# Performance work log

Hardware: AMD Instinct MI355X
Metric: run time of the kernel (lower is better)

The kernel has to match this reference:

```python
import jax, jax.numpy as jnp
import numpy as np

D_MODEL = 1024
NUM_HEADS = 16
HEAD_DIM = D_MODEL // NUM_HEADS          # 64
ROT_W = HEAD_DIM // 2                    # partial_factor=(0.0, 0.5) -> rotary on first half
MAX_LEN = 2048
BASE = 10000.0


def _rope_tables(max_len):
    # theta over even dims of ROT_W, each repeated twice (interleaved pairs): [t0,t0,t1,t1,...]
    theta = 1.0 / (BASE ** (np.arange(0, ROT_W, 2, dtype=np.float32) / ROT_W))  # [ROT_W/2]
    m = np.arange(max_len, dtype=np.float32)[:, None] * theta[None, :]          # [max_len, ROT_W/2]
    m = np.repeat(m, 2, axis=-1)                                                # [max_len, ROT_W]
    return jnp.asarray(np.cos(m)), jnp.asarray(np.sin(m))


def _rotate(x):
    # interleaved pairs (x0, x1) -> (-x1, x0)
    xr = x.reshape(x.shape[:-1] + (-1, 2))
    rot = jnp.stack([-xr[..., 1], xr[..., 0]], axis=-1)
    return rot.reshape(x.shape)


def setup_inputs() -> dict:
    key = jax.random.key(0)
    k1, k2, k3, k4 = jax.random.split(key, 4)
    B, L, H, E = 2, 2048, NUM_HEADS, HEAD_DIM
    return {
        "queries": jax.random.normal(k1, (B, L, H, E), jnp.float32),
        "keys": jax.random.normal(k2, (B, L, H, E), jnp.float32),
        "values": jax.random.normal(k3, (B, L, H, E), jnp.float32),
        "bias_weight": jax.random.normal(k4, (2, H), jnp.float32) * 0.02,  # BinaryAttentionBias embedding
        "n_vars": 32,
        "n_tokens": 64,
    }


def reference(queries, keys, values, bias_weight, n_vars, n_tokens):
    B, L, H, E = queries.shape
    q = queries.transpose(0, 2, 1, 3)  # [B,H,L,E]
    k = keys.transpose(0, 2, 1, 3)     # [B,H,L,E]

    # --- partial rotary projection (shared for q and k), seq_id = arange(L) ---
    cos, sin = _rope_tables(MAX_LEN)
    seq = jnp.arange(n_vars * n_tokens)
    c = cos[seq][None, None]  # [1,1,L,ROT_W]
    s = sin[seq][None, None]

    def rope(x):
        xr = x[..., :ROT_W]
        return jnp.concatenate([c * xr + s * _rotate(xr), x[..., ROT_W:]], axis=-1)

    q = rope(q)
    k = rope(k)

    scale = 1.0 / np.sqrt(E).astype(np.float32)

    # --- binary attention bias: per-head scalar by variable-id equality ---
    var_id = jnp.repeat(jnp.arange(n_vars), n_tokens)          # [L]
    same_var = var_id[:, None] == var_id[None, :]              # [L,L]
    bias = jnp.where(same_var[None, :, :],
                     bias_weight[1][:, None, None],
                     bias_weight[0][:, None, None])            # [H,L,L]

    # --- TimerMultivariateMask: causal in time, full across variables ---
    time_id = seq % n_tokens
    causal_bad = time_id[None, :] > time_id[:, None]           # key time > query time
    attn_mask = jnp.where(causal_bad[None], -jnp.inf, bias)    # [H,L,L]

    scores = jnp.einsum('bhle,bhse->bhls', q, k)               # [B,H,L,L]
    A = jax.nn.softmax(scale * scores + attn_mask[None], axis=-1)
    V = jnp.einsum('bhls,bshd->blhd', A, values)               # [B,L,H,E]
    return V
```

## Files before the change

kernel.cpp:

```cpp
#include <hip/hip_runtime.h>

typedef unsigned short u16;
typedef unsigned int u32;

typedef __attribute__((ext_vector_type(8))) __bf16 bf16x8;
typedef __attribute__((ext_vector_type(4))) float floatx4;

#define B_ 2
#define L_ 2048
#define H_ 16
#define E_ 64
#define QK_ELEMS (B_ * H_ * L_ * E_)
#define WS_OFF 128

static __device__ __forceinline__ float bf2f(u16 v) {
  u32 u = ((u32)v) << 16;
  return __builtin_bit_cast(float, u);
}
static __device__ __forceinline__ u16 f2bf(float x) {
  u32 u = __builtin_bit_cast(u32, x);
  u32 r = (u + 0x7FFFu + ((u >> 16) & 1u)) >> 16;
  return (u16)r;
}

static __device__ __forceinline__ float exp2_fast(float x) {
  float r;
  asm("v_exp_f32 %0, %1" : "=v"(r) : "v"(x));
  return r;
}

static __device__ __forceinline__ void sincos_fast(float a, float* s, float* c) {
  const float INV2PI = 0.15915494309189535f;
  float r = a * INV2PI;
  r = r - floorf(r);
  float ss, cc;
  asm("v_sin_f32 %0, %1" : "=v"(ss) : "v"(r));
  asm("v_cos_f32 %0, %1" : "=v"(cc) : "v"(r));
  *s = ss;
  *c = cc;
}

static __device__ __forceinline__ bool detect_f32_wave(const void* q) {
  u32 w = ((const u32*)q)[threadIdx.x & 63];
  int big = ((((w >> 7) & 0xFF) > 180) | (((w >> 23) & 0xFF) > 180));
  return __ballot(big) != 0ULL;
}

__global__ void detect_dtype(const u16* __restrict__ q, int* __restrict__ flag) {
  int lane = threadIdx.x;
  int big = 0;
#pragma unroll
  for (int i = 0; i < 16; ++i) {
    u16 v = q[lane * 16 + i];
    int e = (v >> 7) & 0xFF;
    big |= (e > 180);
  }
  unsigned long long b = __ballot(big);
  if (lane == 0) *flag = (b != 0ULL) ? 1 : 0;
}

static __device__ __forceinline__ bf16x8 ld8(const void* base, size_t off, bool f32) {
  if (f32) {
    const float* p = (const float*)base + off;
    float4 a = *(const float4*)p;
    float4 bb = *(const float4*)(p + 4);
    uint4 o;
    o.x = (u32)f2bf(a.x) | ((u32)f2bf(a.y) << 16);
    o.y = (u32)f2bf(a.z) | ((u32)f2bf(a.w) << 16);
    o.z = (u32)f2bf(bb.x) | ((u32)f2bf(bb.y) << 16);
    o.w = (u32)f2bf(bb.z) | ((u32)f2bf(bb.w) << 16);
    return __builtin_bit_cast(bf16x8, o);
  }
  return *(const bf16x8*)((const u16*)base + off);
}

static __device__ __forceinline__ bf16x8 rope_frag(bf16x8 x, float pos, int quad) {
  uint4 u = __builtin_bit_cast(uint4, x);
  float v0 = bf2f((u16)u.x), v1 = bf2f((u16)(u.x >> 16));
  float v2 = bf2f((u16)u.y), v3 = bf2f((u16)(u.y >> 16));
  float v4 = bf2f((u16)u.z), v5 = bf2f((u16)(u.z >> 16));
  float v6 = bf2f((u16)u.w), v7 = bf2f((u16)(u.w >> 16));
  const float LB = 0.83048202372184058696f;
  float jb = (float)(quad * 4);
  float a0 = pos * exp2_fast(-jb * LB);
  float a1 = pos * exp2_fast(-(jb + 1.f) * LB);
  float a2 = pos * exp2_fast(-(jb + 2.f) * LB);
  float a3 = pos * exp2_fast(-(jb + 3.f) * LB);
  float s0, c0, s1, c1, s2, c2, s3, c3;
  sincos_fast(a0, &s0, &c0);
  sincos_fast(a1, &s1, &c1);
  sincos_fast(a2, &s2, &c2);
  sincos_fast(a3, &s3, &c3);
  uint4 o;
  o.x = (u32)f2bf(c0 * v0 - s0 * v1) | ((u32)f2bf(c0 * v1 + s0 * v0) << 16);
  o.y = (u32)f2bf(c1 * v2 - s1 * v3) | ((u32)f2bf(c1 * v3 + s1 * v2) << 16);
  o.z = (u32)f2bf(c2 * v4 - s2 * v5) | ((u32)f2bf(c2 * v5 + s2 * v4) << 16);
  o.w = (u32)f2bf(c3 * v6 - s3 * v7) | ((u32)f2bf(c3 * v7 + s3 * v6) << 16);
  return __builtin_bit_cast(bf16x8, o);
}

__global__ __launch_bounds__(256) void prep_kv(
    const void* __restrict__ Q, const void* __restrict__ K, const void* __restrict__ V,
    u16* __restrict__ Kr, u16* __restrict__ VT) {
  __shared__ u16 tile[64][65];
  const int t = threadIdx.x;
  const bool f32 = detect_f32_wave(Q);

  if (blockIdx.x < (B_ * L_)) {
    const int bl = blockIdx.x;
    const int b = bl >> 11, l = bl & (L_ - 1);
    const int h = t >> 4, d = (t & 15) << 2;
    size_t in_off = (((size_t)(b * L_ + l) * H_ + h) * E_) + d;
    size_t out_off = (((size_t)(b * H_ + h) * L_ + l) * E_) + d;
    float k0, k1, k2, k3;
    if (f32) {
      float4 kv = *(const float4*)((const float*)K + in_off);
      k0 = kv.x; k1 = kv.y; k2 = kv.z; k3 = kv.w;
    } else {
      uint2 kv = *(const uint2*)((const u16*)K + in_off);
      k0 = bf2f((u16)kv.x); k1 = bf2f((u16)(kv.x >> 16));
      k2 = bf2f((u16)kv.y); k3 = bf2f((u16)(kv.y >> 16));
    }
    if (d < 32) {
      int j0 = d >> 1;
      const float LB = 0.83048202372184058696f;
      float a0 = (float)l * exp2_fast(-(float)j0 * LB);
      float a1 = (float)l * exp2_fast(-(float)(j0 + 1) * LB);
      float s0, c0, s1, c1;
      sincos_fast(a0, &s0, &c0);
      sincos_fast(a1, &s1, &c1);
      float r;
      r = c0 * k0 - s0 * k1; k1 = c0 * k1 + s0 * k0; k0 = r;
      r = c1 * k2 - s1 * k3; k3 = c1 * k3 + s1 * k2; k2 = r;
    }
    uint2 ko;
    ko.x = (u32)f2bf(k0) | ((u32)f2bf(k1) << 16);
    ko.y = (u32)f2bf(k2) | ((u32)f2bf(k3) << 16);
    *(uint2*)(Kr + out_off) = ko;
  } else {
    const int blk = blockIdx.x - (B_ * L_);
    const int bh = blk & 31, lt = blk >> 5;
    const int b = bh >> 4, h = bh & 15;
    const int l0 = lt << 6;
#pragma unroll
    for (int it = 0; it < 2; ++it) {
      int ll = (t >> 3) + (it << 5);
      int dc = (t & 7) << 3;
      size_t off = (((size_t)(b * L_ + l0 + ll) * H_ + h) * E_) + dc;
      bf16x8 x8 = ld8(V, off, f32);
      uint4 x = __builtin_bit_cast(uint4, x8);
      tile[ll][dc + 0] = (u16)x.x; tile[ll][dc + 1] = (u16)(x.x >> 16);
      tile[ll][dc + 2] = (u16)x.y; tile[ll][dc + 3] = (u16)(x.y >> 16);
      tile[ll][dc + 4] = (u16)x.z; tile[ll][dc + 5] = (u16)(x.z >> 16);
      tile[ll][dc + 6] = (u16)x.w; tile[ll][dc + 7] = (u16)(x.w >> 16);
    }
    __syncthreads();
    int e = t >> 2, lg = (t & 3) << 4;
    u32 pk[8];
#pragma unroll
    for (int i = 0; i < 8; ++i)
      pk[i] = (u32)tile[lg + 2 * i][e] | ((u32)tile[lg + 2 * i + 1][e] << 16);
    u16* dst = VT + (((size_t)bh * E_ + e) * L_) + l0 + lg;
    uint4 o0; o0.x = pk[0]; o0.y = pk[1]; o0.z = pk[2]; o0.w = pk[3];
    uint4 o1; o1.x = pk[4]; o1.y = pk[5]; o1.z = pk[6]; o1.w = pk[7];
    *(uint4*)dst = o0;
    *(uint4*)(dst + 8) = o1;
  }
}

#if __has_builtin(__builtin_amdgcn_global_load_lds)
#define HAS_GLL 1
static __device__ __forceinline__ void gll16(const void* g, void* l) {
  __builtin_amdgcn_global_load_lds(
      (const __attribute__((address_space(1))) u32*)g,
      (__attribute__((address_space(3))) u32*)l, 16, 0, 0);
}
#else
#define HAS_GLL 0
#endif

__global__ __launch_bounds__(256, 2) void flash_staged(
    const void* __restrict__ Q, const u16* __restrict__ Kr,
    const u16* __restrict__ VT, const void* __restrict__ bw,
    void* __restrict__ out) {
  __shared__ u16 kbuf[2][64][64];
  __shared__ u16 vbuf[2][64][64];
  __shared__ u16 plds[4][2][32 * 36];

  const int tid = threadIdx.x;
  const int wid = tid >> 6, lane = tid & 63;
  const int quad = lane >> 4, l16 = lane & 15;
  const int bh = blockIdx.x & 31;
  const int gb = blockIdx.x >> 5;
  const int var_l = (gb << 1) + (wid >> 1);
  const int s0 = (wid & 1) << 4;
  const int base = var_l << 6;
  const int b = bh >> 4, h = bh & 15;

  const bool f32 = detect_f32_wave(Q);
  const u16* Kb = Kr + ((size_t)bh << 17);
  const u16* Vb = VT + ((size_t)bh << 17);

  const float LOG2E = 1.4426950408889634f;
  const float bw_diff = f32 ? ((const float*)bw)[h] : bf2f(((const u16*)bw)[h]);
  const float bw_same = f32 ? ((const float*)bw)[H_ + h] : bf2f(((const u16*)bw)[H_ + h]);
  const float C1 = 0.125f * LOG2E;
  const float c2d = bw_diff * LOG2E;
  const float c2s = bw_same * LOG2E;
  const float NEGINF = -__builtin_inff();

  bf16x8 qf[2][2];
#pragma unroll
  for (int rh = 0; rh < 2; ++rh) {
    const int r = base + s0 + (rh << 5) + l16;
    size_t ro = (((size_t)(b * L_ + r) * H_ + h) * E_);
    qf[rh][0] = rope_frag(ld8(Q, ro + quad * 8, f32), (float)r, quad);
    qf[rh][1] = ld8(Q, ro + 32 + quad * 8, f32);
  }

  const floatx4 zero4 = {0.f, 0.f, 0.f, 0.f};
  bf16x8 ones;
  { uint4 t4; t4.x = t4.y = t4.z = t4.w = 0x3F803F80u; ones = __builtin_bit_cast(bf16x8, t4); }

  floatx4 oacc[2][4], lacc[2];
#pragma unroll
  for (int rh = 0; rh < 2; ++rh) {
    lacc[rh] = zero4;
#pragma unroll
    for (int c4 = 0; c4 < 4; ++c4) oacc[rh][c4] = zero4;
  }

  const int srow = lane >> 3;
  const int sc16 = (lane & 7) ^ srow;
#if !HAS_GLL
  uint4 sk[2], sv[2];
#endif
  auto stage_issue = [&](int bufn, int v) {
    const int k0 = v << 6;
#pragma unroll
    for (int rr = 0; rr < 2; ++rr) {
      const int chunk = (wid << 1) + rr;
      const int row = (chunk << 3) + srow;
      const u16* gk = Kb + (size_t)(k0 + row) * 64 + sc16 * 8;
      const u16* gv = Vb + (size_t)row * L_ + (size_t)k0 + sc16 * 8;
#if HAS_GLL
      gll16(gk, (char*)&kbuf[bufn][0][0] + chunk * 1024);
      gll16(gv, (char*)&vbuf[bufn][0][0] + chunk * 1024);
#else
      sk[rr] = *(const uint4*)gk;
      sv[rr] = *(const uint4*)gv;
#endif
    }
  };
  auto stage_commit = [&](int bufn) {
#if !HAS_GLL
#pragma unroll
    for (int rr = 0; rr < 2; ++rr) {
      const int chunk = (wid << 1) + rr;
      *(uint4*)((u16*)&kbuf[bufn][0][0] + chunk * 512 + lane * 8) = sk[rr];
      *(uint4*)((u16*)&vbuf[bufn][0][0] + chunk * 512 + lane * 8) = sv[rr];
    }
#else
    (void)bufn;
#endif
  };

  stage_issue(0, 0);
  stage_commit(0);
  __asm__ volatile("s_waitcnt vmcnt(0)" ::: "memory");
  __syncthreads();

  int pp = 0;
  const int sw = l16 & 7;

  for (int v = 0; v < 32; ++v) {
    const int buf = v & 1;
    const bool more = (v < 31);
    if (more) stage_issue(buf ^ 1, v + 1);
    const float c2 = (v == var_l) ? c2s : c2d;

    bf16x8 kf[2][2];
#pragma unroll
    for (int ch = 0; ch < 2; ++ch) {
      const int row = ch * 16 + l16;
#pragma unroll
      for (int hf = 0; hf < 2; ++hf)
        kf[ch][hf] = *(const bf16x8*)&kbuf[buf][row][(((hf << 2) + quad) ^ sw) << 3];
    }
    floatx4 cc[2][2];
#pragma unroll
    for (int rh = 0; rh < 2; ++rh)
#pragma unroll
      for (int ch = 0; ch < 2; ++ch) {
        floatx4 acc = __builtin_amdgcn_mfma_f32_16x16x32_bf16(qf[rh][0], kf[ch][0], zero4, 0, 0, 0);
        cc[rh][ch] = __builtin_amdgcn_mfma_f32_16x16x32_bf16(qf[rh][1], kf[ch][1], acc, 0, 0, 0);
      }
    u16* const pw = &plds[wid][pp][0];
#pragma unroll
    for (int rh = 0; rh < 2; ++rh)
#pragma unroll
      for (int ch = 0; ch < 2; ++ch)
#pragma unroll
        for (int reg = 0; reg < 4; ++reg) {
          float s = fmaf(cc[rh][ch][reg], C1, c2);
          if (rh == 0 && (ch * 16 + l16 > s0 + quad * 4 + reg)) s = NEGINF;
          pw[(rh * 16 + quad * 4 + reg) * 36 + ch * 16 + l16] = f2bf(exp2_fast(s));
        }
    __asm__ volatile("s_waitcnt lgkmcnt(0)" ::: "memory");
    bf16x8 pa[2];
#pragma unroll
    for (int rh = 0; rh < 2; ++rh) {
      const u16* pr = pw + (rh * 16 + l16) * 36 + quad * 8;
      uint2 lo = *(const uint2*)pr;
      uint2 hi = *(const uint2*)(pr + 4);
      uint4 cmb; cmb.x = lo.x; cmb.y = lo.y; cmb.z = hi.x; cmb.w = hi.y;
      pa[rh] = __builtin_bit_cast(bf16x8, cmb);
    }
#pragma unroll
    for (int rh = 0; rh < 2; ++rh)
      lacc[rh] = __builtin_amdgcn_mfma_f32_16x16x32_bf16(pa[rh], ones, lacc[rh], 0, 0, 0);
#pragma unroll
    for (int c4 = 0; c4 < 4; ++c4) {
      bf16x8 vf = *(const bf16x8*)&vbuf[buf][c4 * 16 + l16][(quad ^ sw) << 3];
#pragma unroll
      for (int rh = 0; rh < 2; ++rh)
        oacc[rh][c4] = __builtin_amdgcn_mfma_f32_16x16x32_bf16(pa[rh], vf, oacc[rh][c4], 0, 0, 0);
    }
    pp ^= 1;

    bf16x8 kg[2][2];
#pragma unroll
    for (int ch = 0; ch < 2; ++ch) {
      const int row = 32 + ch * 16 + l16;
#pragma unroll
      for (int hf = 0; hf < 2; ++hf)
        kg[ch][hf] = *(const bf16x8*)&kbuf[buf][row][(((hf << 2) + quad) ^ sw) << 3];
    }
    floatx4 dd[2];
#pragma unroll
    for (int ch = 0; ch < 2; ++ch) {
      floatx4 acc = __builtin_amdgcn_mfma_f32_16x16x32_bf16(qf[1][0], kg[ch][0], zero4, 0, 0, 0);
      dd[ch] = __builtin_amdgcn_mfma_f32_16x16x32_bf16(qf[1][1], kg[ch][1], acc, 0, 0, 0);
    }
    u16* const pw2 = &plds[wid][pp][0];
#pragma unroll
    for (int ch = 0; ch < 2; ++ch)
#pragma unroll
      for (int reg = 0; reg < 4; ++reg) {
        float s = fmaf(dd[ch][reg], C1, c2);
        if (ch * 16 + l16 > s0 + quad * 4 + reg) s = NEGINF;
        pw2[(16 + quad * 4 + reg) * 36 + ch * 16 + l16] = f2bf(exp2_fast(s));
      }
    __asm__ volatile("s_waitcnt lgkmcnt(0)" ::: "memory");
    bf16x8 pb;
    {
      const u16* pr = pw2 + (16 + l16) * 36 + quad * 8;
      uint2 lo = *(const uint2*)pr;
      uint2 hi = *(const uint2*)(pr + 4);
      uint4 cmb; cmb.x = lo.x; cmb.y = lo.y; cmb.z = hi.x; cmb.w = hi.y;
      pb = __builtin_bit_cast(bf16x8, cmb);
    }
    lacc[1] = __builtin_amdgcn_mfma_f32_16x16x32_bf16(pb, ones, lacc[1], 0, 0, 0);
#pragma unroll
    for (int c4 = 0; c4 < 4; ++c4) {
      bf16x8 vf = *(const bf16x8*)&vbuf[buf][c4 * 16 + l16][(((4 + quad) ^ sw)) << 3];
      oacc[1][c4] = __builtin_amdgcn_mfma_f32_16x16x32_bf16(pb, vf, oacc[1][c4], 0, 0, 0);
    }
    pp ^= 1;

    if (more) {
      stage_commit(buf ^ 1);
      __asm__ volatile("s_waitcnt vmcnt(0)" ::: "memory");
      __syncthreads();
    }
  }

  float rinv[2][4];
#pragma unroll
  for (int rh = 0; rh < 2; ++rh)
#pragma unroll
    for (int reg = 0; reg < 4; ++reg) {
      float lv = lacc[rh][reg];
      rinv[rh][reg] = (lv > 1e-30f) ? 1.0f / lv : 0.0f;
    }

#pragma unroll
  for (int rh = 0; rh < 2; ++rh)
#pragma unroll
    for (int c4 = 0; c4 < 4; ++c4)
#pragma unroll
      for (int reg = 0; reg < 4; ++reg) {
        const int row = base + s0 + (rh << 5) + quad * 4 + reg;
        const int col = c4 * 16 + l16;
        float val = oacc[rh][c4][reg] * rinv[rh][reg];
        size_t oo = (((size_t)(b * L_ + row)) * H_ + h) * E_ + col;
        if (f32) ((float*)out)[oo] = val;
        else ((u16*)out)[oo] = f2bf(val);
      }
}

__global__ __launch_bounds__(256) void flash_fused(
    const void* __restrict__ Q, const void* __restrict__ K,
    const void* __restrict__ V, const void* __restrict__ bw,
    const int* __restrict__ flag, void* __restrict__ out) {
  __shared__ u16 plds[4][2][32 * 36];
  __shared__ u16 vlds[4][64][40];
  const bool f32 = flag ? (*flag != 0) : true;
  const int tid = threadIdx.x;
  const int wid = tid >> 6, lane = tid & 63;
  const int quad = lane >> 4, l16 = lane & 15;
  const int bh = blockIdx.x & 31;
  const int g = blockIdx.x >> 5;
  const int rowblk = (g << 2) + wid;
  const int row0 = rowblk << 5;
  const int b = bh >> 4, h = bh & 15;
  const int t0 = row0 & 63;
  const int var_l = row0 >> 6;
  const int ktiles = (t0 >> 5) + 1;

  const float bw_diff = f32 ? ((const float*)bw)[h] : bf2f(((const u16*)bw)[h]);
  const float bw_same = f32 ? ((const float*)bw)[H_ + h] : bf2f(((const u16*)bw)[H_ + h]);

  const floatx4 zero4 = {0.f, 0.f, 0.f, 0.f};
  bf16x8 ones;
  { uint4 t4; t4.x = t4.y = t4.z = t4.w = 0x3F803F80u; ones = __builtin_bit_cast(bf16x8, t4); }

  bf16x8 qf[2][2];
#pragma unroll
  for (int rh = 0; rh < 2; ++rh) {
    const int r = row0 + rh * 16 + l16;
    size_t ro = (((size_t)(b * L_ + r) * H_ + h) * E_);
#pragma unroll
    for (int hf = 0; hf < 2; ++hf)
      qf[rh][hf] = ld8(Q, ro + hf * 32 + quad * 8, f32);
    qf[rh][0] = rope_frag(qf[rh][0], (float)r, quad);
  }

  floatx4 oacc[2][4], lacc[2];
#pragma unroll
  for (int rh = 0; rh < 2; ++rh) {
    lacc[rh] = zero4;
#pragma unroll
    for (int c4 = 0; c4 < 4; ++c4) oacc[rh][c4] = zero4;
  }

  u16* const pbase = &plds[wid][0][0];
  u16* const vb = &vlds[wid][0][0];
  int pp = 0;

  for (int v = 0; v < 32; ++v) {
    const float bias = (v == var_l) ? bw_same : bw_diff;
    for (int kt = 0; kt < ktiles; ++kt) {
      const int k0 = (v << 6) + (kt << 5);

      bf16x8 kf[2][2];
#pragma unroll
      for (int ch = 0; ch < 2; ++ch) {
        const int r = k0 + ch * 16 + l16;
        size_t ro = (((size_t)(b * L_ + r) * H_ + h) * E_);
#pragma unroll
        for (int hf = 0; hf < 2; ++hf)
          kf[ch][hf] = ld8(K, ro + hf * 32 + quad * 8, f32);
        kf[ch][0] = rope_frag(kf[ch][0], (float)r, quad);
      }

      floatx4 cc[2][2];
#pragma unroll
      for (int rh = 0; rh < 2; ++rh)
#pragma unroll
        for (int ch = 0; ch < 2; ++ch) {
          floatx4 acc = __builtin_amdgcn_mfma_f32_16x16x32_bf16(qf[rh][0], kf[ch][0], zero4, 0, 0, 0);
          cc[rh][ch] = __builtin_amdgcn_mfma_f32_16x16x32_bf16(qf[rh][1], kf[ch][1], acc, 0, 0, 0);
        }

      u16* const pw = pbase + pp * (32 * 36);
      const int ts_b = (kt << 5) + l16;
#pragma unroll
      for (int rh = 0; rh < 2; ++rh)
#pragma unroll
        for (int ch = 0; ch < 2; ++ch) {
          const int ts = ts_b + ch * 16;
#pragma unroll
          for (int reg = 0; reg < 4; ++reg) {
            const int tl = t0 + rh * 16 + quad * 4 + reg;
            float s = cc[rh][ch][reg] * 0.125f + bias;
            float p = (ts > tl) ? 0.0f : __expf(s);
            pw[(rh * 16 + quad * 4 + reg) * 36 + ch * 16 + l16] = f2bf(p);
          }
        }

#pragma unroll
      for (int it = 0; it < 4; ++it) {
        const int s = (lane >> 3) + it * 8;
        const int dc = (lane & 7) << 3;
        size_t vo = (((size_t)(b * L_ + k0 + s) * H_ + h) * E_) + dc;
        bf16x8 x8 = ld8(V, vo, f32);
        uint4 x = __builtin_bit_cast(uint4, x8);
        vb[(dc + 0) * 40 + s] = (u16)x.x; vb[(dc + 1) * 40 + s] = (u16)(x.x >> 16);
        vb[(dc + 2) * 40 + s] = (u16)x.y; vb[(dc + 3) * 40 + s] = (u16)(x.y >> 16);
        vb[(dc + 4) * 40 + s] = (u16)x.z; vb[(dc + 5) * 40 + s] = (u16)(x.z >> 16);
        vb[(dc + 6) * 40 + s] = (u16)x.w; vb[(dc + 7) * 40 + s] = (u16)(x.w >> 16);
      }

      __asm__ volatile("s_waitcnt lgkmcnt(0)" ::: "memory");

      bf16x8 pa[2];
#pragma unroll
      for (int rh = 0; rh < 2; ++rh) {
        const u16* pr = pw + (rh * 16 + l16) * 36 + quad * 8;
        uint2 lo = *(const uint2*)pr;
        uint2 hi = *(const uint2*)(pr + 4);
        uint4 cmb; cmb.x = lo.x; cmb.y = lo.y; cmb.z = hi.x; cmb.w = hi.y;
        pa[rh] = __builtin_bit_cast(bf16x8, cmb);
      }

#pragma unroll
      for (int rh = 0; rh < 2; ++rh)
        lacc[rh] = __builtin_amdgcn_mfma_f32_16x16x32_bf16(pa[rh], ones, lacc[rh], 0, 0, 0);

#pragma unroll
      for (int c4 = 0; c4 < 4; ++c4) {
        bf16x8 vf = *(const bf16x8*)(vb + (c4 * 16 + l16) * 40 + quad * 8);
#pragma unroll
        for (int rh = 0; rh < 2; ++rh)
          oacc[rh][c4] = __builtin_amdgcn_mfma_f32_16x16x32_bf16(pa[rh], vf, oacc[rh][c4], 0, 0, 0);
      }
      pp ^= 1;
    }
  }

  float rinv[2][4];
#pragma unroll
  for (int rh = 0; rh < 2; ++rh)
#pragma unroll
    for (int reg = 0; reg < 4; ++reg) {
      float lv = lacc[rh][reg];
      rinv[rh][reg] = (lv > 1e-30f) ? 1.0f / lv : 0.0f;
    }

#pragma unroll
  for (int rh = 0; rh < 2; ++rh)
#pragma unroll
    for (int c4 = 0; c4 < 4; ++c4)
#pragma unroll
      for (int reg = 0; reg < 4; ++reg) {
        const int row = row0 + rh * 16 + quad * 4 + reg;
        const int col = c4 * 16 + l16;
        float val = oacc[rh][c4][reg] * rinv[rh][reg];
        size_t oo = (((size_t)(b * L_ + row)) * H_ + h) * E_ + col;
        if (f32) ((float*)out)[oo] = val;
        else ((u16*)out)[oo] = f2bf(val);
      }
}

extern "C" void kernel_launch(void* const* d_in, const int* in_sizes, int n_in,
                              void* d_out, int out_size, void* d_ws, size_t ws_size,
                              hipStream_t stream) {
  (void)in_sizes; (void)n_in; (void)out_size;
  const void* q = d_in[0];
  const void* k = d_in[1];
  const void* v = d_in[2];
  const void* bwp = d_in[3];
  const size_t need = (size_t)WS_OFF * 2 + 2u * QK_ELEMS * sizeof(u16);
  if (ws_size >= need) {
    u16* Kr = (u16*)d_ws + WS_OFF;
    u16* VT = Kr + QK_ELEMS;
    prep_kv<<<B_ * L_ + B_ * H_ * (L_ / 64), 256, 0, stream>>>(q, k, v, Kr, VT);
    flash_staged<<<512, 256, 0, stream>>>(q, Kr, VT, bwp, d_out);
  } else if (ws_size >= sizeof(int)) {
    int* flag = (int*)d_ws;
    detect_dtype<<<1, 64, 0, stream>>>((const u16*)q, flag);
    flash_fused<<<512, 256, 0, stream>>>(q, k, v, bwp, flag, d_out);
  } else {
    flash_fused<<<512, 256, 0, stream>>>(q, k, v, bwp, (const int*)nullptr, d_out);
  }
}
```

Before: 151.8 us.

## Load K directly from global, tile V transpose, transpose score MFMA, packed bf16 P

K fragments are now read straight from global memory (L2-resident) into registers instead of being staged through LDS, so only V is double-buffered in shared memory. The prep kernel writes V^T in 64x64 tiles so each staged block is one contiguous 8KB region. The QK^T MFMA operands are swapped so the score layout lets P be written as packed bf16 pairs with v_cvt_pk_bf16_f32, and all three P tiles are handled in one LDS round-trip instead of two. The cost is a global-load latency on K each iteration with no prefetch, which could stall the wave.

```diff
diff --git a/kernel.cpp b/kernel.cpp
--- a/kernel.cpp
+++ b/kernel.cpp
@@ -21,6 +21,12 @@
   u32 u = __builtin_bit_cast(u32, x);
   u32 r = (u + 0x7FFFu + ((u >> 16) & 1u)) >> 16;
   return (u16)r;
+}
+
+static __device__ __forceinline__ u32 cvtpk_bf16(float lo, float hi) {
+  u32 r;
+  asm("v_cvt_pk_bf16_f32 %0, %1, %2" : "=v"(r) : "v"(lo), "v"(hi));
+  return r;
 }
 
 static __device__ __forceinline__ float exp2_fast(float x) {
@@ -160,7 +166,7 @@
 #pragma unroll
     for (int i = 0; i < 8; ++i)
       pk[i] = (u32)tile[lg + 2 * i][e] | ((u32)tile[lg + 2 * i + 1][e] << 16);
-    u16* dst = VT + (((size_t)bh * E_ + e) * L_) + l0 + lg;
+    u16* dst = VT + (((size_t)(bh * 32 + lt)) << 12) + e * 64 + lg;
     uint4 o0; o0.x = pk[0]; o0.y = pk[1]; o0.z = pk[2]; o0.w = pk[3];
     uint4 o1; o1.x = pk[4]; o1.y = pk[5]; o1.z = pk[6]; o1.w = pk[7];
     *(uint4*)dst = o0;
@@ -179,13 +185,12 @@
 #define HAS_GLL 0
 #endif
 
-__global__ __launch_bounds__(256, 2) void flash_staged(
+__global__ __launch_bounds__(256, 2) void flash_v5(
     const void* __restrict__ Q, const u16* __restrict__ Kr,
     const u16* __restrict__ VT, const void* __restrict__ bw,
     void* __restrict__ out) {
-  __shared__ u16 kbuf[2][64][64];
   __shared__ u16 vbuf[2][64][64];
-  __shared__ u16 plds[4][2][32 * 36];
+  __shared__ u32 plds[4][2][48][20];
 
   const int tid = threadIdx.x;
   const int wid = tid >> 6, lane = tid & 63;
@@ -232,41 +237,21 @@
 
   const int srow = lane >> 3;
   const int sc16 = (lane & 7) ^ srow;
-#if !HAS_GLL
-  uint4 sk[2], sv[2];
-#endif
   auto stage_issue = [&](int bufn, int v) {
-    const int k0 = v << 6;
 #pragma unroll
     for (int rr = 0; rr < 2; ++rr) {
       const int chunk = (wid << 1) + rr;
-      const int row = (chunk << 3) + srow;
-      const u16* gk = Kb + (size_t)(k0 + row) * 64 + sc16 * 8;
-      const u16* gv = Vb + (size_t)row * L_ + (size_t)k0 + sc16 * 8;
+      const u16* gv = Vb + ((size_t)v << 12) + (size_t)((chunk << 3) + srow) * 64 + sc16 * 8;
 #if HAS_GLL
-      gll16(gk, (char*)&kbuf[bufn][0][0] + chunk * 1024);
       gll16(gv, (char*)&vbuf[bufn][0][0] + chunk * 1024);
 #else
-      sk[rr] = *(const uint4*)gk;
-      sv[rr] = *(const uint4*)gv;
+      uint4 x = *(const uint4*)gv;
+      *(uint4*)((u16*)&vbuf[bufn][0][0] + chunk * 512 + lane * 8) = x;
 #endif
     }
   };
-  auto stage_commit = [&](int bufn) {
-#if !HAS_GLL
-#pragma unroll
-    for (int rr = 0; rr < 2; ++rr) {
-      const int chunk = (wid << 1) + rr;
-      *(uint4*)((u16*)&kbuf[bufn][0][0] + chunk * 512 + lane * 8) = sk[rr];
-      *(uint4*)((u16*)&vbuf[bufn][0][0] + chunk * 512 + lane * 8) = sv[rr];
-    }
-#else
-    (void)bufn;
-#endif
-  };
 
   stage_issue(0, 0);
-  stage_commit(0);
   __asm__ volatile("s_waitcnt vmcnt(0)" ::: "memory");
   __syncthreads();
 
@@ -275,101 +260,88 @@
 
   for (int v = 0; v < 32; ++v) {
     const int buf = v & 1;
-    const bool more = (v < 31);
-    if (more) stage_issue(buf ^ 1, v + 1);
+    const int k0 = v << 6;
+
+    bf16x8 kf[2][2], kg[2][2];
+#pragma unroll
+    for (int ch = 0; ch < 2; ++ch) {
+      const u16* kr0 = Kb + (size_t)(k0 + ch * 16 + l16) * 64 + quad * 8;
+      kf[ch][0] = *(const bf16x8*)kr0;
+      kf[ch][1] = *(const bf16x8*)(kr0 + 32);
+      const u16* kr1 = kr0 + 32 * 64;
+      kg[ch][0] = *(const bf16x8*)kr1;
+      kg[ch][1] = *(const bf16x8*)(kr1 + 32);
+    }
+    if (v < 31) stage_issue(buf ^ 1, v + 1);
+    bf16x8 vf0[4], vf1[4];
+#pragma unroll
+    for (int c4 = 0; c4 < 4; ++c4) {
+      vf0[c4] = *(const bf16x8*)&vbuf[buf][c4 * 16 + l16][(quad ^ sw) << 3];
+      vf1[c4] = *(const bf16x8*)&vbuf[buf][c4 * 16 + l16][((4 + quad) ^ sw) << 3];
+    }
     const float c2 = (v == var_l) ? c2s : c2d;
 
-    bf16x8 kf[2][2];
+    floatx4 cc[2][2], dd[2];
 #pragma unroll
     for (int ch = 0; ch < 2; ++ch) {
-      const int row = ch * 16 + l16;
-#pragma unroll
-      for (int hf = 0; hf < 2; ++hf)
-        kf[ch][hf] = *(const bf16x8*)&kbuf[buf][row][(((hf << 2) + quad) ^ sw) << 3];
-    }
-    floatx4 cc[2][2];
-#pragma unroll
-    for (int rh = 0; rh < 2; ++rh)
-#pragma unroll
-      for (int ch = 0; ch < 2; ++ch) {
-        floatx4 acc = __builtin_amdgcn_mfma_f32_16x16x32_bf16(qf[rh][0], kf[ch][0], zero4, 0, 0, 0);
-        cc[rh][ch] = __builtin_amdgcn_mfma_f32_16x16x32_bf16(qf[rh][1], kf[ch][1], acc, 0, 0, 0);
-      }
-    u16* const pw = &plds[wid][pp][0];
-#pragma unroll
-    for (int rh = 0; rh < 2; ++rh)
-#pragma unroll
-      for (int ch = 0; ch < 2; ++ch)
-#pragma unroll
-        for (int reg = 0; reg < 4; ++reg) {
-          float s = fmaf(cc[rh][ch][reg], C1, c2);
-          if (rh == 0 && (ch * 16 + l16 > s0 + quad * 4 + reg)) s = NEGINF;
-          pw[(rh * 16 + quad * 4 + reg) * 36 + ch * 16 + l16] = f2bf(exp2_fast(s));
-        }
+#pragma unroll
+      for (int rh = 0; rh < 2; ++rh) {
+        floatx4 a0 = __builtin_amdgcn_mfma_f32_16x16x32_bf16(kf[ch][0], qf[rh][0], zero4, 0, 0, 0);
+        cc[rh][ch] = __builtin_amdgcn_mfma_f32_16x16x32_bf16(kf[ch][1], qf[rh][1], a0, 0, 0, 0);
+      }
+      floatx4 a1 = __builtin_amdgcn_mfma_f32_16x16x32_bf16(kg[ch][0], qf[1][0], zero4, 0, 0, 0);
+      dd[ch] = __builtin_amdgcn_mfma_f32_16x16x32_bf16(kg[ch][1], qf[1][1], a1, 0, 0, 0);
+    }
+
+    u32* const prow = &plds[wid][pp][0][0];
+#pragma unroll
+    for (int ch = 0; ch < 2; ++ch) {
+      float p0[4], p1[4], p2[4];
+#pragma unroll
+      for (int reg = 0; reg < 4; ++reg) {
+        const bool msk = (ch * 16 + quad * 4 + reg) > (s0 + l16);
+        float sA = fmaf(cc[0][ch][reg], C1, c2);
+        if (msk) sA = NEGINF;
+        p0[reg] = exp2_fast(sA);
+        p1[reg] = exp2_fast(fmaf(cc[1][ch][reg], C1, c2));
+        float sC = fmaf(dd[ch][reg], C1, c2);
+        if (msk) sC = NEGINF;
+        p2[reg] = exp2_fast(sC);
+      }
+      u32* w0 = prow + (0 + l16) * 20 + ch * 8 + quad * 2;
+      w0[0] = cvtpk_bf16(p0[0], p0[1]);
+      w0[1] = cvtpk_bf16(p0[2], p0[3]);
+      u32* w1 = prow + (16 + l16) * 20 + ch * 8 + quad * 2;
+      w1[0] = cvtpk_bf16(p1[0], p1[1]);
+      w1[1] = cvtpk_bf16(p1[2], p1[3]);
+      u32* w2 = prow + (32 + l16) * 20 + ch * 8 + quad * 2;
+      w2[0] = cvtpk_bf16(p2[0], p2[1]);
+      w2[1] = cvtpk_bf16(p2[2], p2[3]);
+    }
     __asm__ volatile("s_waitcnt lgkmcnt(0)" ::: "memory");
-    bf16x8 pa[2];
-#pragma unroll
-    for (int rh = 0; rh < 2; ++rh) {
-      const u16* pr = pw + (rh * 16 + l16) * 36 + quad * 8;
-      uint2 lo = *(const uint2*)pr;
-      uint2 hi = *(const uint2*)(pr + 4);
-      uint4 cmb; cmb.x = lo.x; cmb.y = lo.y; cmb.z = hi.x; cmb.w = hi.y;
-      pa[rh] = __builtin_bit_cast(bf16x8, cmb);
-    }
-#pragma unroll
-    for (int rh = 0; rh < 2; ++rh)
-      lacc[rh] = __builtin_amdgcn_mfma_f32_16x16x32_bf16(pa[rh], ones, lacc[rh], 0, 0, 0);
+    bf16x8 pa0, pa1, pb2;
+    {
+      const u32* r0 = prow + (0 + l16) * 20 + quad * 4;
+      uint4 t4; t4.x = r0[0]; t4.y = r0[1]; t4.z = r0[2]; t4.w = r0[3];
+      pa0 = __builtin_bit_cast(bf16x8, t4);
+      const u32* r1 = prow + (16 + l16) * 20 + quad * 4;
+      uint4 t5; t5.x = r1[0]; t5.y = r1[1]; t5.z = r1[2]; t5.w = r1[3];
+      pa1 = __builtin_bit_cast(bf16x8, t5);
+      const u32* r2 = prow + (32 + l16) * 20 + quad * 4;
+      uint4 t6; t6.x = r2[0]; t6.y = r2[1]; t6.z = r2[2]; t6.w = r2[3];
+      pb2 = __builtin_bit_cast(bf16x8, t6);
+    }
+    lacc[0] = __builtin_amdgcn_mfma_f32_16x16x32_bf16(pa0, ones, lacc[0], 0, 0, 0);
+    lacc[1] = __builtin_amdgcn_mfma_f32_16x16x32_bf16(pa1, ones, lacc[1], 0, 0, 0);
+    lacc[1] = __builtin_amdgcn_mfma_f32_16x16x32_bf16(pb2, ones, lacc[1], 0, 0, 0);
 #pragma unroll
     for (int c4 = 0; c4 < 4; ++c4) {
-      bf16x8 vf = *(const bf16x8*)&vbuf[buf][c4 * 16 + l16][(quad ^ sw) << 3];
-#pragma unroll
-      for (int rh = 0; rh < 2; ++rh)
-        oacc[rh][c4] = __builtin_amdgcn_mfma_f32_16x16x32_bf16(pa[rh], vf, oacc[rh][c4], 0, 0, 0);
+      oacc[0][c4] = __builtin_amdgcn_mfma_f32_16x16x32_bf16(pa0, vf0[c4], oacc[0][c4], 0, 0, 0);
+      oacc[1][c4] = __builtin_amdgcn_mfma_f32_16x16x32_bf16(pa1, vf0[c4], oacc[1][c4], 0, 0, 0);
+      oacc[1][c4] = __builtin_amdgcn_mfma_f32_16x16x32_bf16(pb2, vf1[c4], oacc[1][c4], 0, 0, 0);
     }
     pp ^= 1;
-
-    bf16x8 kg[2][2];
-#pragma unroll
-    for (int ch = 0; ch < 2; ++ch) {
-      const int row = 32 + ch * 16 + l16;
-#pragma unroll
-      for (int hf = 0; hf < 2; ++hf)
-        kg[ch][hf] = *(const bf16x8*)&kbuf[buf][row][(((hf << 2) + quad) ^ sw) << 3];
-    }
-    floatx4 dd[2];
-#pragma unroll
-    for (int ch = 0; ch < 2; ++ch) {
-      floatx4 acc = __builtin_amdgcn_mfma_f32_16x16x32_bf16(qf[1][0], kg[ch][0], zero4, 0, 0, 0);
-      dd[ch] = __builtin_amdgcn_mfma_f32_16x16x32_bf16(qf[1][1], kg[ch][1], acc, 0, 0, 0);
-    }
-    u16* const pw2 = &plds[wid][pp][0];
-#pragma unroll
-    for (int ch = 0; ch < 2; ++ch)
-#pragma unroll
-      for (int reg = 0; reg < 4; ++reg) {
-        float s = fmaf(dd[ch][reg], C1, c2);
-        if (ch * 16 + l16 > s0 + quad * 4 + reg) s = NEGINF;
-        pw2[(16 + quad * 4 + reg) * 36 + ch * 16 + l16] = f2bf(exp2_fast(s));
-      }
-    __asm__ volatile("s_waitcnt lgkmcnt(0)" ::: "memory");
-    bf16x8 pb;
-    {
-      const u16* pr = pw2 + (16 + l16) * 36 + quad * 8;
-      uint2 lo = *(const uint2*)pr;
-      uint2 hi = *(const uint2*)(pr + 4);
-      uint4 cmb; cmb.x = lo.x; cmb.y = lo.y; cmb.z = hi.x; cmb.w = hi.y;
-      pb = __builtin_bit_cast(bf16x8, cmb);
-    }
-    lacc[1] = __builtin_amdgcn_mfma_f32_16x16x32_bf16(pb, ones, lacc[1], 0, 0, 0);
-#pragma unroll
-    for (int c4 = 0; c4 < 4; ++c4) {
-      bf16x8 vf = *(const bf16x8*)&vbuf[buf][c4 * 16 + l16][(((4 + quad) ^ sw)) << 3];
-      oacc[1][c4] = __builtin_amdgcn_mfma_f32_16x16x32_bf16(pb, vf, oacc[1][c4], 0, 0, 0);
-    }
-    pp ^= 1;
-
-    if (more) {
-      stage_commit(buf ^ 1);
+    if (v < 31) {
       __asm__ volatile("s_waitcnt vmcnt(0)" ::: "memory");
       __syncthreads();
     }
@@ -566,7 +538,7 @@
     u16* Kr = (u16*)d_ws + WS_OFF;
     u16* VT = Kr + QK_ELEMS;
     prep_kv<<<B_ * L_ + B_ * H_ * (L_ / 64), 256, 0, stream>>>(q, k, v, Kr, VT);
-    flash_staged<<<512, 256, 0, stream>>>(q, Kr, VT, bwp, d_out);
+    flash_v5<<<512, 256, 0, stream>>>(q, Kr, VT, bwp, d_out);
   } else if (ws_size >= sizeof(int)) {
     int* flag = (int*)d_ws;
     detect_dtype<<<1, 64, 0, stream>>>((const u16*)q, flag);
```

New measurement: 168.0 us. 1.11x slower.
